# Kernel optimization log

Measured on AMD Instinct MI355X. Metric: run time of the kernel, lower is better.

## Reference

```python
import jax, jax.numpy as jnp
import numpy as np

SEQ = 1024  # hardcoded target length in the original module


def _build_target(indexes):
    """Vectorized circular piecewise-cosine target, [B, SEQ] float32.

    For each position p, find the segment [m_i, m_{i+1}) (circular) it lies in;
    value = cos((p - m_i) * 2*pi / seg_len) * 0.5 + 0.5.
    """
    m = jnp.sort(indexes, axis=1)  # [B, 4], original sorts in-place
    p = jnp.arange(SEQ)            # [SEQ]
    # seg = index of largest breakpoint <= p; -1 means wrap segment (use 3)
    seg = jnp.sum(m[:, :, None] <= p[None, None, :], axis=1) - 1  # [B, SEQ]
    seg = jnp.where(seg < 0, 3, seg)
    start = jnp.take_along_axis(m, seg, axis=1)                 # [B, SEQ]
    nxt = jnp.take_along_axis(m, (seg + 1) % 4, axis=1)         # [B, SEQ]
    n = (nxt - start) % SEQ                                     # circular segment length
    k = (p[None, :] - start) % SEQ                              # offset within segment
    ang = k.astype(jnp.float32) * (2.0 * jnp.pi) / n.astype(jnp.float32)
    return jnp.cos(ang) * 0.5 + 0.5


def setup_inputs() -> dict:
    key = jax.random.key(0)
    k1, k2 = jax.random.split(key)
    B = 32768
    outputs = jax.random.normal(k1, (B, 1, SEQ), dtype=jnp.float32)
    # strictly increasing breakpoints in [0, 1024): sorted base + arange(4)
    base = jnp.sort(jax.random.randint(k2, (B, 4), 0, SEQ - 3), axis=1)
    indexes = base + jnp.arange(4)
    return {"outputs": outputs, "indexes": indexes}


def reference(outputs, indexes):
    B = outputs.shape[0]
    N = outputs.shape[2]
    tgt = _build_target(indexes)  # [B, SEQ]
    loss = jnp.sum(jnp.square(outputs[:, 0, :] - tgt))
    return loss / (B * N)
```

## Files before the change

kernel.cpp:

```cpp
#include <hip/hip_runtime.h>

#define SEQ  1024
#define SEQM 1023
#define RPB  16

__device__ __forceinline__ float block_reduce_sum(float v) {
    #pragma unroll
    for (int o = 32; o > 0; o >>= 1) v += __shfl_down(v, o, 64);
    __shared__ float s[16];
    const int lane = threadIdx.x & 63;
    const int w    = threadIdx.x >> 6;
    if (lane == 0) s[w] = v;
    __syncthreads();
    const int nw = blockDim.x >> 6;
    if (w == 0) {
        v = (lane < nw) ? s[lane] : 0.0f;
        #pragma unroll
        for (int o = 8; o > 0; o >>= 1) v += __shfl_down(v, o, 64);
    }
    return v;
}

__device__ __forceinline__ float sq_elem(float valm, float pf, float pfw,
                                         float4 C, float4 Bv, float acc) {
    float rev = fmaf(pfw, C.w, -Bv.w);
    const float r0 = fmaf(pf, C.x, -Bv.x);
    const float r1 = fmaf(pf, C.y, -Bv.y);
    const float r2 = fmaf(pf, C.z, -Bv.z);
    const float r3 = fmaf(pf, C.w, -Bv.w);
    rev = (r0 >= 0.0f) ? r0 : rev;
    rev = (r1 >= 0.0f) ? r1 : rev;
    rev = (r2 >= 0.0f) ? r2 : rev;
    rev = (r3 >= 0.0f) ? r3 : rev;
    const float d = fmaf(__builtin_amdgcn_cosf(rev), -0.5f, valm);
    return fmaf(d, d, acc);
}

template <bool WEIGHTED>
__device__ __forceinline__ float do_row(float4 v, float4 C, float4 Bv, float w,
                                        float pf0, float pf1, float pf2, float pf3,
                                        float pw0, float pw1, float pw2, float pw3,
                                        float acc) {
    float r = WEIGHTED ? 0.0f : acc;
    r = sq_elem(v.x - 0.5f, pf0, pw0, C, Bv, r);
    r = sq_elem(v.y - 0.5f, pf1, pw1, C, Bv, r);
    r = sq_elem(v.z - 0.5f, pf2, pw2, C, Bv, r);
    r = sq_elem(v.w - 0.5f, pf3, pw3, C, Bv, r);
    return WEIGHTED ? fmaf(r, w, acc) : r;
}

__global__ __launch_bounds__(256) void criterion_partial(
        const float* __restrict__ outputs,
        const int*   __restrict__ indexes,
        float*       __restrict__ part,
        int B) {
    __shared__ float4 sC[RPB];
    __shared__ float4 sB[RPB];
    __shared__ float  sW[RPB];

    const int tid  = threadIdx.x;
    const int row0 = blockIdx.x * RPB;
    const bool full = (row0 + RPB <= B);

    if (tid < RPB) {
        int r = row0 + tid;
        sW[tid] = (r < B) ? 1.0f : 0.0f;
        r = (r < B) ? r : (B - 1);
        const int4 mi = *reinterpret_cast<const int4*>(indexes + (size_t)r * 4);
        int m0 = mi.x, m1 = mi.y, m2 = mi.z, m3 = mi.w;
        int t;
        if (m0 > m1) { t = m0; m0 = m1; m1 = t; }
        if (m2 > m3) { t = m2; m2 = m3; m3 = t; }
        if (m0 > m2) { t = m0; m0 = m2; m2 = t; }
        if (m1 > m3) { t = m1; m1 = m3; m3 = t; }
        if (m1 > m2) { t = m1; m1 = m2; m2 = t; }
        const float c0 = __builtin_amdgcn_rcpf((float)((m1 - m0) & SEQM));
        const float c1 = __builtin_amdgcn_rcpf((float)((m2 - m1) & SEQM));
        const float c2 = __builtin_amdgcn_rcpf((float)((m3 - m2) & SEQM));
        const float c3 = __builtin_amdgcn_rcpf((float)((m0 - m3) & SEQM));
        sC[tid] = make_float4(c0, c1, c2, c3);
        sB[tid] = make_float4((float)m0 * c0, (float)m1 * c1,
                              (float)m2 * c2, (float)m3 * c3);
    }
    __syncthreads();

    const int   pb  = tid * 4;
    const float pf0 = (float)pb,        pf1 = pf0 + 1.0f;
    const float pf2 = pf0 + 2.0f,       pf3 = pf0 + 3.0f;
    const float pw0 = pf0 + 1024.0f,    pw1 = pw0 + 1.0f;
    const float pw2 = pw0 + 2.0f,       pw3 = pw0 + 3.0f;
    float acc = 0.0f;

    if (full) {
        const float* rowp = outputs + (size_t)row0 * SEQ + pb;
        #pragma unroll 1
        for (int rr = 0; rr < RPB; rr += 4) {
            const float4 v0 = *reinterpret_cast<const float4*>(rowp + (rr + 0) * SEQ);
            const float4 v1 = *reinterpret_cast<const float4*>(rowp + (rr + 1) * SEQ);
            const float4 v2 = *reinterpret_cast<const float4*>(rowp + (rr + 2) * SEQ);
            const float4 v3 = *reinterpret_cast<const float4*>(rowp + (rr + 3) * SEQ);
            acc = do_row<false>(v0, sC[rr + 0], sB[rr + 0], 1.0f,
                                pf0, pf1, pf2, pf3, pw0, pw1, pw2, pw3, acc);
            acc = do_row<false>(v1, sC[rr + 1], sB[rr + 1], 1.0f,
                                pf0, pf1, pf2, pf3, pw0, pw1, pw2, pw3, acc);
            acc = do_row<false>(v2, sC[rr + 2], sB[rr + 2], 1.0f,
                                pf0, pf1, pf2, pf3, pw0, pw1, pw2, pw3, acc);
            acc = do_row<false>(v3, sC[rr + 3], sB[rr + 3], 1.0f,
                                pf0, pf1, pf2, pf3, pw0, pw1, pw2, pw3, acc);
        }
    } else {
        #pragma unroll 1
        for (int rr = 0; rr < RPB; ++rr) {
            const int r = (row0 + rr < B) ? (row0 + rr) : (B - 1);
            const float4 v = *reinterpret_cast<const float4*>(
                outputs + (size_t)r * SEQ + pb);
            acc = do_row<true>(v, sC[rr], sB[rr], sW[rr],
                               pf0, pf1, pf2, pf3, pw0, pw1, pw2, pw3, acc);
        }
    }

    const float bsum = block_reduce_sum(acc);
    if (tid == 0) part[blockIdx.x] = bsum;
}

__global__ __launch_bounds__(256) void criterion_final(
        const float* __restrict__ part,
        float*       __restrict__ out,
        int npart, float inv_bn) {
    float v = 0.0f;
    for (int i = threadIdx.x; i < npart; i += 256) v += part[i];
    const float s = block_reduce_sum(v);
    if (threadIdx.x == 0) out[0] = s * inv_bn;
}

extern "C" void kernel_launch(void* const* d_in, const int* in_sizes, int n_in,
                              void* d_out, int out_size, void* d_ws, size_t ws_size,
                              hipStream_t stream) {
    const float* outputs = (const float*)d_in[0];
    const int*   indexes = (const int*)d_in[1];
    float* out  = (float*)d_out;
    float* part = (float*)d_ws;

    const int total = in_sizes[0];
    const int B = total / SEQ;
    const int npart = (B + RPB - 1) / RPB;

    criterion_partial<<<npart, 256, 0, stream>>>(outputs, indexes, part, B);
    criterion_final<<<1, 256, 0, stream>>>(part, out, npart,
                                           (float)(1.0 / (double)total));
}
```

Measured before the change: 29.98 us.

## Fuse final reduction via last-block atomic counter and prefetch next rows

Merges the two-kernel reduction into one kernel: each block writes its partial sum, bumps a global counter atomically, and whichever block arrives last reduces all partials. The main loop now loads the next four rows before computing the current four, overlapping memory latency with the cosine math. The wrap-segment offset is now computed as r3 plus a precomputed 1024*C.w instead of a separate FMA with extra registers. Risks include the counter in workspace never being zeroed: it relies on modulo wraparound across calls, which breaks if the workspace starts non-zero. Holding prefetched data also raises register pressure.

```diff
diff --git a/kernel.cpp b/kernel.cpp
--- a/kernel.cpp
+++ b/kernel.cpp
@@ -21,42 +21,44 @@
     return v;
 }
 
-__device__ __forceinline__ float sq_elem(float valm, float pf, float pfw,
-                                         float4 C, float4 Bv, float acc) {
-    float rev = fmaf(pfw, C.w, -Bv.w);
+__device__ __forceinline__ float sq_elem(float val, float pf,
+                                         float4 C, float4 Bv, float kw,
+                                         float acc) {
     const float r0 = fmaf(pf, C.x, -Bv.x);
     const float r1 = fmaf(pf, C.y, -Bv.y);
     const float r2 = fmaf(pf, C.z, -Bv.z);
     const float r3 = fmaf(pf, C.w, -Bv.w);
+    float rev = r3 + kw;
     rev = (r0 >= 0.0f) ? r0 : rev;
     rev = (r1 >= 0.0f) ? r1 : rev;
     rev = (r2 >= 0.0f) ? r2 : rev;
     rev = (r3 >= 0.0f) ? r3 : rev;
-    const float d = fmaf(__builtin_amdgcn_cosf(rev), -0.5f, valm);
+    const float d = fmaf(__builtin_amdgcn_cosf(rev), -0.5f, val - 0.5f);
     return fmaf(d, d, acc);
 }
 
-template <bool WEIGHTED>
-__device__ __forceinline__ float do_row(float4 v, float4 C, float4 Bv, float w,
-                                        float pf0, float pf1, float pf2, float pf3,
-                                        float pw0, float pw1, float pw2, float pw3,
-                                        float acc) {
-    float r = WEIGHTED ? 0.0f : acc;
-    r = sq_elem(v.x - 0.5f, pf0, pw0, C, Bv, r);
-    r = sq_elem(v.y - 0.5f, pf1, pw1, C, Bv, r);
-    r = sq_elem(v.z - 0.5f, pf2, pw2, C, Bv, r);
-    r = sq_elem(v.w - 0.5f, pf3, pw3, C, Bv, r);
-    return WEIGHTED ? fmaf(r, w, acc) : r;
+__device__ __forceinline__ float do_row(float4 v, float4 C, float4 Bv,
+                                        float pf0, float pf1, float pf2,
+                                        float pf3, float acc) {
+    const float kw = 1024.0f * C.w;
+    acc = sq_elem(v.x, pf0, C, Bv, kw, acc);
+    acc = sq_elem(v.y, pf1, C, Bv, kw, acc);
+    acc = sq_elem(v.z, pf2, C, Bv, kw, acc);
+    acc = sq_elem(v.w, pf3, C, Bv, kw, acc);
+    return acc;
 }
 
-__global__ __launch_bounds__(256) void criterion_partial(
+__global__ __launch_bounds__(256) void criterion_fused(
         const float* __restrict__ outputs,
         const int*   __restrict__ indexes,
         float*       __restrict__ part,
-        int B) {
+        unsigned int* __restrict__ counter,
+        float*       __restrict__ out,
+        int B, int npart, float inv_bn) {
     __shared__ float4 sC[RPB];
     __shared__ float4 sB[RPB];
     __shared__ float  sW[RPB];
+    __shared__ unsigned int s_old;
 
     const int tid  = threadIdx.x;
     const int row0 = blockIdx.x * RPB;
@@ -85,52 +87,58 @@
     __syncthreads();
 
     const int   pb  = tid * 4;
-    const float pf0 = (float)pb,        pf1 = pf0 + 1.0f;
-    const float pf2 = pf0 + 2.0f,       pf3 = pf0 + 3.0f;
-    const float pw0 = pf0 + 1024.0f,    pw1 = pw0 + 1.0f;
-    const float pw2 = pw0 + 2.0f,       pw3 = pw0 + 3.0f;
+    const float pf0 = (float)pb, pf1 = pf0 + 1.0f;
+    const float pf2 = pf0 + 2.0f, pf3 = pf0 + 3.0f;
     float acc = 0.0f;
 
     if (full) {
         const float* rowp = outputs + (size_t)row0 * SEQ + pb;
+        float4 a0 = *reinterpret_cast<const float4*>(rowp + 0 * SEQ);
+        float4 a1 = *reinterpret_cast<const float4*>(rowp + 1 * SEQ);
+        float4 a2 = *reinterpret_cast<const float4*>(rowp + 2 * SEQ);
+        float4 a3 = *reinterpret_cast<const float4*>(rowp + 3 * SEQ);
         #pragma unroll 1
-        for (int rr = 0; rr < RPB; rr += 4) {
-            const float4 v0 = *reinterpret_cast<const float4*>(rowp + (rr + 0) * SEQ);
-            const float4 v1 = *reinterpret_cast<const float4*>(rowp + (rr + 1) * SEQ);
-            const float4 v2 = *reinterpret_cast<const float4*>(rowp + (rr + 2) * SEQ);
-            const float4 v3 = *reinterpret_cast<const float4*>(rowp + (rr + 3) * SEQ);
-            acc = do_row<false>(v0, sC[rr + 0], sB[rr + 0], 1.0f,
-                                pf0, pf1, pf2, pf3, pw0, pw1, pw2, pw3, acc);
-            acc = do_row<false>(v1, sC[rr + 1], sB[rr + 1], 1.0f,
-                                pf0, pf1, pf2, pf3, pw0, pw1, pw2, pw3, acc);
-            acc = do_row<false>(v2, sC[rr + 2], sB[rr + 2], 1.0f,
-                                pf0, pf1, pf2, pf3, pw0, pw1, pw2, pw3, acc);
-            acc = do_row<false>(v3, sC[rr + 3], sB[rr + 3], 1.0f,
-                                pf0, pf1, pf2, pf3, pw0, pw1, pw2, pw3, acc);
+        for (int rr = 4; rr < RPB; rr += 4) {
+            const float4 b0 = *reinterpret_cast<const float4*>(rowp + (rr + 0) * SEQ);
+            const float4 b1 = *reinterpret_cast<const float4*>(rowp + (rr + 1) * SEQ);
+            const float4 b2 = *reinterpret_cast<const float4*>(rowp + (rr + 2) * SEQ);
+            const float4 b3 = *reinterpret_cast<const float4*>(rowp + (rr + 3) * SEQ);
+            acc = do_row(a0, sC[rr - 4], sB[rr - 4], pf0, pf1, pf2, pf3, acc);
+            acc = do_row(a1, sC[rr - 3], sB[rr - 3], pf0, pf1, pf2, pf3, acc);
+            acc = do_row(a2, sC[rr - 2], sB[rr - 2], pf0, pf1, pf2, pf3, acc);
+            acc = do_row(a3, sC[rr - 1], sB[rr - 1], pf0, pf1, pf2, pf3, acc);
+            a0 = b0; a1 = b1; a2 = b2; a3 = b3;
         }
+        acc = do_row(a0, sC[RPB - 4], sB[RPB - 4], pf0, pf1, pf2, pf3, acc);
+        acc = do_row(a1, sC[RPB - 3], sB[RPB - 3], pf0, pf1, pf2, pf3, acc);
+        acc = do_row(a2, sC[RPB - 2], sB[RPB - 2], pf0, pf1, pf2, pf3, acc);
+        acc = do_row(a3, sC[RPB - 1], sB[RPB - 1], pf0, pf1, pf2, pf3, acc);
     } else {
         #pragma unroll 1
         for (int rr = 0; rr < RPB; ++rr) {
             const int r = (row0 + rr < B) ? (row0 + rr) : (B - 1);
             const float4 v = *reinterpret_cast<const float4*>(
                 outputs + (size_t)r * SEQ + pb);
-            acc = do_row<true>(v, sC[rr], sB[rr], sW[rr],
-                               pf0, pf1, pf2, pf3, pw0, pw1, pw2, pw3, acc);
+            const float rs = do_row(v, sC[rr], sB[rr], pf0, pf1, pf2, pf3, 0.0f);
+            acc = fmaf(rs, sW[rr], acc);
         }
     }
 
     const float bsum = block_reduce_sum(acc);
-    if (tid == 0) part[blockIdx.x] = bsum;
-}
+    if (tid == 0) {
+        part[blockIdx.x] = bsum;
+        __threadfence();
+        s_old = atomicAdd(counter, 1u);
+    }
+    __syncthreads();
 
-__global__ __launch_bounds__(256) void criterion_final(
-        const float* __restrict__ part,
-        float*       __restrict__ out,
-        int npart, float inv_bn) {
-    float v = 0.0f;
-    for (int i = threadIdx.x; i < npart; i += 256) v += part[i];
-    const float s = block_reduce_sum(v);
-    if (threadIdx.x == 0) out[0] = s * inv_bn;
+    if ((s_old + 1u) % (unsigned)npart == 0u) {
+        __threadfence();
+        float v = 0.0f;
+        for (int i = tid; i < npart; i += 256) v += part[i];
+        const float s = block_reduce_sum(v);
+        if (tid == 0) out[0] = s * inv_bn;
+    }
 }
 
 extern "C" void kernel_launch(void* const* d_in, const int* in_sizes, int n_in,
@@ -140,12 +148,12 @@
     const int*   indexes = (const int*)d_in[1];
     float* out  = (float*)d_out;
     float* part = (float*)d_ws;
-
     const int total = in_sizes[0];
     const int B = total / SEQ;
     const int npart = (B + RPB - 1) / RPB;
+    unsigned int* counter = (unsigned int*)(part + npart);
 
-    criterion_partial<<<npart, 256, 0, stream>>>(outputs, indexes, part, B);
-    criterion_final<<<1, 256, 0, stream>>>(part, out, npart,
-                                           (float)(1.0 / (double)total));
+    criterion_fused<<<npart, 256, 0, stream>>>(outputs, indexes, part, counter,
+                                               out, B, npart,
+                                               (float)(1.0 / (double)total));
 }
```

After: 77.21 us. 158% more time.

## Use packed FP32 FMA, unsigned-min segment select, and software-pipelined row loads

Applied to the files above, without the earlier changes.

Computes the segment-relative phases two at a time with v_pk_fma_f32 and negated precomputed offsets. The four compare/select steps are replaced by an unsigned integer min over the float bit patterns, which picks the smallest non-negative phase because negative floats have the sign bit set. The row loop is software-pipelined so the next group of four rows is loaded while the current group is processed. The aim is fewer VALU instructions per element and load latency hidden behind compute, at the cost of more registers and inline asm the compiler cannot schedule around.

```diff
diff --git a/kernel.cpp b/kernel.cpp
--- a/kernel.cpp
+++ b/kernel.cpp
@@ -3,6 +3,19 @@
 #define SEQ  1024
 #define SEQM 1023
 #define RPB  16
+
+typedef float f32x2 __attribute__((ext_vector_type(2)));
+
+__device__ __forceinline__ f32x2 pk_fma(f32x2 a, f32x2 b, f32x2 c) {
+    f32x2 d;
+    asm("v_pk_fma_f32 %0, %1, %2, %3" : "=v"(d) : "v"(a), "v"(b), "v"(c));
+    return d;
+}
+__device__ __forceinline__ f32x2 pk_add(f32x2 a, f32x2 b) {
+    f32x2 d;
+    asm("v_pk_add_f32 %0, %1, %2" : "=v"(d) : "v"(a), "v"(b));
+    return d;
+}
 
 __device__ __forceinline__ float block_reduce_sum(float v) {
     #pragma unroll
@@ -21,32 +34,39 @@
     return v;
 }
 
-__device__ __forceinline__ float sq_elem(float valm, float pf, float pfw,
-                                         float4 C, float4 Bv, float acc) {
-    float rev = fmaf(pfw, C.w, -Bv.w);
-    const float r0 = fmaf(pf, C.x, -Bv.x);
-    const float r1 = fmaf(pf, C.y, -Bv.y);
-    const float r2 = fmaf(pf, C.z, -Bv.z);
-    const float r3 = fmaf(pf, C.w, -Bv.w);
-    rev = (r0 >= 0.0f) ? r0 : rev;
-    rev = (r1 >= 0.0f) ? r1 : rev;
-    rev = (r2 >= 0.0f) ? r2 : rev;
-    rev = (r3 >= 0.0f) ? r3 : rev;
+__device__ __forceinline__ float sq_elem(float valm, f32x2 pf2, float pfw,
+                                         f32x2 C01, f32x2 C23,
+                                         f32x2 NB01, f32x2 NB23,
+                                         float c3, float nb3, float acc) {
+    const f32x2 r01 = pk_fma(pf2, C01, NB01);
+    const f32x2 r23 = pk_fma(pf2, C23, NB23);
+    const float rw  = fmaf(pfw, c3, nb3);
+    const unsigned u =
+        min(min(__float_as_uint(r01.x), __float_as_uint(r01.y)),
+            min(min(__float_as_uint(r23.x), __float_as_uint(r23.y)),
+                __float_as_uint(rw)));
+    const float rev = __uint_as_float(u);
     const float d = fmaf(__builtin_amdgcn_cosf(rev), -0.5f, valm);
     return fmaf(d, d, acc);
 }
 
-template <bool WEIGHTED>
-__device__ __forceinline__ float do_row(float4 v, float4 C, float4 Bv, float w,
-                                        float pf0, float pf1, float pf2, float pf3,
-                                        float pw0, float pw1, float pw2, float pw3,
+__device__ __forceinline__ float do_row(float4 v, float4 C, float4 NB,
+                                        const f32x2* pf2, const float* pw,
                                         float acc) {
-    float r = WEIGHTED ? 0.0f : acc;
-    r = sq_elem(v.x - 0.5f, pf0, pw0, C, Bv, r);
-    r = sq_elem(v.y - 0.5f, pf1, pw1, C, Bv, r);
-    r = sq_elem(v.z - 0.5f, pf2, pw2, C, Bv, r);
-    r = sq_elem(v.w - 0.5f, pf3, pw3, C, Bv, r);
-    return WEIGHTED ? fmaf(r, w, acc) : r;
+    f32x2 C01;  C01.x = C.x;   C01.y = C.y;
+    f32x2 C23;  C23.x = C.z;   C23.y = C.w;
+    f32x2 NB01; NB01.x = NB.x; NB01.y = NB.y;
+    f32x2 NB23; NB23.x = NB.z; NB23.y = NB.w;
+    f32x2 half2; half2.x = -0.5f; half2.y = -0.5f;
+    f32x2 v01;  v01.x = v.x;   v01.y = v.y;
+    f32x2 v23;  v23.x = v.z;   v23.y = v.w;
+    const f32x2 vm01 = pk_add(v01, half2);
+    const f32x2 vm23 = pk_add(v23, half2);
+    acc = sq_elem(vm01.x, pf2[0], pw[0], C01, C23, NB01, NB23, C.w, NB.w, acc);
+    acc = sq_elem(vm01.y, pf2[1], pw[1], C01, C23, NB01, NB23, C.w, NB.w, acc);
+    acc = sq_elem(vm23.x, pf2[2], pw[2], C01, C23, NB01, NB23, C.w, NB.w, acc);
+    acc = sq_elem(vm23.y, pf2[3], pw[3], C01, C23, NB01, NB23, C.w, NB.w, acc);
+    return acc;
 }
 
 __global__ __launch_bounds__(256) void criterion_partial(
@@ -55,7 +75,7 @@
         float*       __restrict__ part,
         int B) {
     __shared__ float4 sC[RPB];
-    __shared__ float4 sB[RPB];
+    __shared__ float4 sNB[RPB];
     __shared__ float  sW[RPB];
 
     const int tid  = threadIdx.x;
@@ -78,44 +98,54 @@
         const float c1 = __builtin_amdgcn_rcpf((float)((m2 - m1) & SEQM));
         const float c2 = __builtin_amdgcn_rcpf((float)((m3 - m2) & SEQM));
         const float c3 = __builtin_amdgcn_rcpf((float)((m0 - m3) & SEQM));
-        sC[tid] = make_float4(c0, c1, c2, c3);
-        sB[tid] = make_float4((float)m0 * c0, (float)m1 * c1,
-                              (float)m2 * c2, (float)m3 * c3);
+        sC[tid]  = make_float4(c0, c1, c2, c3);
+        sNB[tid] = make_float4(-(float)m0 * c0, -(float)m1 * c1,
+                               -(float)m2 * c2, -(float)m3 * c3);
     }
     __syncthreads();
 
     const int   pb  = tid * 4;
-    const float pf0 = (float)pb,        pf1 = pf0 + 1.0f;
-    const float pf2 = pf0 + 2.0f,       pf3 = pf0 + 3.0f;
-    const float pw0 = pf0 + 1024.0f,    pw1 = pw0 + 1.0f;
-    const float pw2 = pw0 + 2.0f,       pw3 = pw0 + 3.0f;
+    const float pf0 = (float)pb;
+    f32x2 pf2[4];
+    float pw[4];
+    #pragma unroll
+    for (int j = 0; j < 4; ++j) {
+        const float pf = pf0 + (float)j;
+        pf2[j].x = pf; pf2[j].y = pf;
+        pw[j] = pf + 1024.0f;
+    }
     float acc = 0.0f;
 
     if (full) {
         const float* rowp = outputs + (size_t)row0 * SEQ + pb;
+        float4 a0 = *reinterpret_cast<const float4*>(rowp + 0 * SEQ);
+        float4 a1 = *reinterpret_cast<const float4*>(rowp + 1 * SEQ);
+        float4 a2 = *reinterpret_cast<const float4*>(rowp + 2 * SEQ);
+        float4 a3 = *reinterpret_cast<const float4*>(rowp + 3 * SEQ);
         #pragma unroll 1
-        for (int rr = 0; rr < RPB; rr += 4) {
-            const float4 v0 = *reinterpret_cast<const float4*>(rowp + (rr + 0) * SEQ);
-            const float4 v1 = *reinterpret_cast<const float4*>(rowp + (rr + 1) * SEQ);
-            const float4 v2 = *reinterpret_cast<const float4*>(rowp + (rr + 2) * SEQ);
-            const float4 v3 = *reinterpret_cast<const float4*>(rowp + (rr + 3) * SEQ);
-            acc = do_row<false>(v0, sC[rr + 0], sB[rr + 0], 1.0f,
-                                pf0, pf1, pf2, pf3, pw0, pw1, pw2, pw3, acc);
-            acc = do_row<false>(v1, sC[rr + 1], sB[rr + 1], 1.0f,
-                                pf0, pf1, pf2, pf3, pw0, pw1, pw2, pw3, acc);
-            acc = do_row<false>(v2, sC[rr + 2], sB[rr + 2], 1.0f,
-                                pf0, pf1, pf2, pf3, pw0, pw1, pw2, pw3, acc);
-            acc = do_row<false>(v3, sC[rr + 3], sB[rr + 3], 1.0f,
-                                pf0, pf1, pf2, pf3, pw0, pw1, pw2, pw3, acc);
+        for (int rr = 4; rr < RPB; rr += 4) {
+            const float4 b0 = *reinterpret_cast<const float4*>(rowp + (rr + 0) * SEQ);
+            const float4 b1 = *reinterpret_cast<const float4*>(rowp + (rr + 1) * SEQ);
+            const float4 b2 = *reinterpret_cast<const float4*>(rowp + (rr + 2) * SEQ);
+            const float4 b3 = *reinterpret_cast<const float4*>(rowp + (rr + 3) * SEQ);
+            acc = do_row(a0, sC[rr - 4], sNB[rr - 4], pf2, pw, acc);
+            acc = do_row(a1, sC[rr - 3], sNB[rr - 3], pf2, pw, acc);
+            acc = do_row(a2, sC[rr - 2], sNB[rr - 2], pf2, pw, acc);
+            acc = do_row(a3, sC[rr - 1], sNB[rr - 1], pf2, pw, acc);
+            a0 = b0; a1 = b1; a2 = b2; a3 = b3;
         }
+        acc = do_row(a0, sC[RPB - 4], sNB[RPB - 4], pf2, pw, acc);
+        acc = do_row(a1, sC[RPB - 3], sNB[RPB - 3], pf2, pw, acc);
+        acc = do_row(a2, sC[RPB - 2], sNB[RPB - 2], pf2, pw, acc);
+        acc = do_row(a3, sC[RPB - 1], sNB[RPB - 1], pf2, pw, acc);
     } else {
         #pragma unroll 1
         for (int rr = 0; rr < RPB; ++rr) {
             const int r = (row0 + rr < B) ? (row0 + rr) : (B - 1);
             const float4 v = *reinterpret_cast<const float4*>(
                 outputs + (size_t)r * SEQ + pb);
-            acc = do_row<true>(v, sC[rr], sB[rr], sW[rr],
-                               pf0, pf1, pf2, pf3, pw0, pw1, pw2, pw3, acc);
+            const float rs = do_row(v, sC[rr], sNB[rr], pf2, pw, 0.0f);
+            acc = fmaf(rs, sW[rr], acc);
         }
     }
 
```

Measured after the change: 29.67 us. No clear change (-1.0%).
